# Kernel tuning notes

Measured on AMD Instinct MI355X. Metric: run time of the kernel, lower is better.

Reference implementation:

```python
import jax, jax.numpy as jnp
import numpy as np

N, E = 25000, 400000
HID, EDGE_F, DIM, HEADS, ADY = 128, 16, 3, 8, 64
INNER = int(1.25 * HID)          # 160
MSG_F = 2 * HID + EDGE_F + 1     # 273 (e3, relaxed=False -> 1 distance feature)


def silu(x):
    return x * jax.nn.sigmoid(x)


def ada_ln(x, y, W, b):
    # LayerNorm (no affine) + FiLM conditioning from y
    mu = jnp.mean(x, axis=-1, keepdims=True)
    var = jnp.var(x, axis=-1, keepdims=True)
    xn = (x - mu) * jax.lax.rsqrt(var + 1e-5)
    scale, shift = jnp.split(y @ W + b, 2, axis=-1)
    return xn * (1.0 + scale) + shift


def setup_inputs() -> dict:
    key = jax.random.key(0)
    ks = jax.random.split(key, 32)
    rn = lambda k, shp, s=0.05: (jax.random.normal(k, shp, jnp.float32) * s)
    inp = {
        'h': jax.random.normal(ks[0], (N, HID), jnp.float32),
        'coords': jax.random.normal(ks[1], (N, DIM), jnp.float32),
        'a': jax.random.normal(ks[2], (E, EDGE_F), jnp.float32),
        'y': jax.random.normal(ks[3], (N, ADY), jnp.float32),
        'res': jnp.zeros((N, HID), jnp.float32),
        'src': jax.random.randint(ks[4], (E,), 0, N, jnp.int32),
        'dst': jax.random.randint(ks[5], (E,), 0, N, jnp.int32),
        # edge MLP
        'We1': rn(ks[6], (MSG_F, INNER)), 'be1': jnp.zeros((INNER,), jnp.float32),
        'We2': rn(ks[7], (INNER, INNER)), 'be2': jnp.zeros((INNER,), jnp.float32),
        # coord head (xavier gain 0.001 -> tiny init)
        'Wc': rn(ks[8], (INNER, 1), 0.001),
        # attention/value/output heads
        'Wv': rn(ks[9], (INNER, HID)),
        'Wa': rn(ks[10], (INNER, HEADS)),
        'Wo': rn(ks[11], (HID, HID)),
        # node MLP
        'Wn1': rn(ks[12], (HID, INNER)), 'bn1': jnp.zeros((INNER,), jnp.float32),
        'Wn2': rn(ks[13], (INNER, HID)), 'bn2': jnp.zeros((HID,), jnp.float32),
        # adaptive LayerNorms (FiLM from y)
        'Wf1': rn(ks[14], (ADY, 2 * HID)), 'bf1': jnp.zeros((2 * HID,), jnp.float32),
        'Wf2': rn(ks[15], (ADY, 2 * HID)), 'bf2': jnp.zeros((2 * HID,), jnp.float32),
    }
    return inp


def reference(h, coords, a, y, res, src, dst,
              We1, be1, We2, be2, Wc, Wv, Wa, Wo,
              Wn1, bn1, Wn2, bn2, Wf1, bf1, Wf2, bf2):
    n = h.shape[0]
    heads = Wa.shape[1]
    # --- distance features (e3, relaxed=False): radial only ---
    xs, xd = coords[src], coords[dst]          # [E, 3]
    diffs = xs - xd
    radials = jnp.sum(diffs * diffs, axis=-1, keepdims=True)  # [E, 1]
    # --- edge MLP on gathered features ---
    f = jnp.concatenate([h[src], h[dst], radials, a], axis=-1)  # [E, 273]
    m = silu(f @ We1 + be1)
    m = silu(m @ We2 + be2)                    # [E, inner]
    # --- coordinate messages + scatter-sum to dst ---
    msg_x = (m @ Wc) * diffs / (jnp.sqrt(radials + 1e-5) + 1.0)  # [E, 3]
    coords_out = coords + jax.ops.segment_sum(msg_x, dst, num_segments=n)
    # --- edge softmax over incoming edges per dst node ---
    logits = m @ Wa                             # [E, heads]
    mx = jax.ops.segment_max(logits, dst, num_segments=n)
    ex = jnp.exp(logits - mx[dst])
    den = jax.ops.segment_sum(ex, dst, num_segments=n)
    w = ex / den[dst]                           # [E, heads]
    # --- weighted value aggregation ---
    vals = (m @ Wv).reshape(-1, heads, HID // heads) * w[:, :, None]
    h_agg = jax.ops.segment_sum(vals, dst, num_segments=n).reshape(n, HID)
    f2 = h_agg @ Wo
    res1 = res + f2
    h1 = ada_ln(h + f2, y, Wf1, bf1)
    f3 = silu(h1 @ Wn1 + bn1) @ Wn2 + bn2
    res2 = res1 + f3
    h2 = ada_ln(h1 + f3, y, Wf2, bf2)
    return (h2, coords_out, res2)
```

## Files before the change

kernel.cpp:

```cpp
#include <hip/hip_runtime.h>
#include <math.h>

#define N_NODES 25000
#define N_EDGES 400000
#define HID 128
#define EDGE_F 16
#define ADY 64
#define INNER 160
#define MSG_F 273
#define HEADS 8

#define OUT_CRD (N_NODES * HID)
#define OUT_RES (N_NODES * (HID + 3))

#define FLAG_OFF 0
#define DEN_OFF  256
#define CACC_OFF 800256
#define HAGG_OFF 1100288
#define HBF_OFF  13900288
#define YBF_OFF  20300288
#define BIAS_OFF 23500288
#define BW_OFF   23502592
#define MEMSET_BYTES 13900288

typedef unsigned short u16;
typedef unsigned int u32;
typedef unsigned long long u64;
typedef __attribute__((ext_vector_type(8))) short short8;
typedef __attribute__((ext_vector_type(4))) float f32x4;

__device__ __forceinline__ float bf2f(u16 v) {
    union { u32 u; float f; } x; x.u = ((u32)v) << 16; return x.f;
}
__device__ __forceinline__ u16 f2bf(float f) {
    union { float ff; u32 u; } x; x.ff = f;
    u32 u = x.u;
    u32 rounding = 0x7FFFu + ((u >> 16) & 1u);
    u += rounding;
    return (u16)(u >> 16);
}
__device__ __forceinline__ float silu(float z) {
    z = fminf(fmaxf(z, -30000.f), 30000.f);
    return z / (1.0f + __expf(-z));
}

template<bool F32> __device__ __forceinline__ float ldg1(const void* p, size_t i) {
    if (F32) return ((const float*)p)[i];
    return bf2f(((const u16*)p)[i]);
}
template<bool F32> __device__ __forceinline__ void stg1(void* p, size_t i, float v) {
    if (F32) ((float*)p)[i] = v;
    else     ((u16*)p)[i] = f2bf(v);
}
__device__ __forceinline__ float ldany(const void* p, size_t i, bool f32) {
    return f32 ? ((const float*)p)[i] : bf2f(((const u16*)p)[i]);
}
__device__ __forceinline__ void wave_lds_fence() {
    __builtin_amdgcn_wave_barrier();
    __builtin_amdgcn_s_waitcnt(0xc07f);
    __builtin_amdgcn_wave_barrier();
}

struct CvtArgs {
    const void* src[8];
    u64 dstoff[8];
    int n[8];
};
struct BwArgs {
    const void* We1; const void* We2; const void* Wv; const void* Wa;
    const void* Wc;  const void* Wo;  const void* Wn1; const void* Wn2;
    const void* Wf1; const void* Wf2;
    u64 b1, b2, b3, b4, b5, b6, b7, b8;
};

__global__ __launch_bounds__(256)
void preproc_kernel(const void* hsrc, int* flag, char* ws, CvtArgs args, BwArgs bwa)
{
    __shared__ float red[256];
    __shared__ int sflag;
    const int t = threadIdx.x;
    {
        const u16* p = (const u16*)hsrc;
        float mx = 0.f;
        for (int i = 0; i < 8; i++) {
            int idx = (t * 8 + i) * 97;
            float v = fabsf(bf2f(p[idx * 2]));
            mx = fmaxf(mx, v);
        }
        red[t] = mx;
        __syncthreads();
        for (int s = 128; s > 0; s >>= 1) {
            if (t < s) red[t] = fmaxf(red[t], red[t + s]);
            __syncthreads();
        }
        if (t == 0) {
            sflag = (red[0] > 1e10f || red[0] == 0.f) ? 1 : 0;
            if (blockIdx.x == 0) flag[0] = sflag;
        }
        __syncthreads();
    }
    const bool f32 = (sflag != 0);
    const int g = blockIdx.x * 256 + t;
    const int stride = gridDim.x * 256;

    for (int ten = 0; ten < 8; ten++) {
        const void* s = args.src[ten];
        u16* d = (u16*)(ws + args.dstoff[ten]);
        const int n = args.n[ten];
        if (f32) {
            const float* sf = (const float*)s;
            for (int i = g; i < n; i += stride) d[i] = f2bf(sf[i]);
        } else {
            const u16* su = (const u16*)s;
            for (int i = g; i < n; i += stride) d[i] = su[i];
        }
    }

    u16* b1 = (u16*)(ws + bwa.b1);
    u16* b2 = (u16*)(ws + bwa.b2);
    u16* b3 = (u16*)(ws + bwa.b3);
    u16* b4 = (u16*)(ws + bwa.b4);
    u16* b5 = (u16*)(ws + bwa.b5);
    u16* b6 = (u16*)(ws + bwa.b6);
    u16* b7 = (u16*)(ws + bwa.b7);
    u16* b8 = (u16*)(ws + bwa.b8);
    for (int i = g; i < 5*2*10*512; i += stride) {
        int tt = i >> 9, r = i & 511, l = r >> 3, j = r & 7;
        int c = tt / 20, ks = (tt / 10) % 2, nt = tt % 10;
        int k = c*64 + ks*32 + (l >> 4)*8 + j;
        int n = nt*16 + (l & 15);
        float v = 0.f;
        if (k < MSG_F)      v = ldany(bwa.We1, (size_t)k*INNER + n, f32);
        else if (k == 273)  v = ldany(bwa.We1, (size_t)256*INNER + n, f32);
        b1[i] = f2bf(v);
    }
    for (int i = g; i < 5*10*512; i += stride) {
        int tt = i >> 9, r = i & 511, l = r >> 3, j = r & 7;
        int k5 = tt / 10, nt = tt % 10;
        int k = k5*32 + (l >> 4)*8 + j;
        int n = nt*16 + (l & 15);
        b2[i] = f2bf(ldany(bwa.We2, (size_t)k*INNER + n, f32));
    }
    for (int i = g; i < 5*9*512; i += stride) {
        int tt = i >> 9, r = i & 511, l = r >> 3, j = r & 7;
        int k5 = tt / 9, nt = tt % 9;
        int k = k5*32 + (l >> 4)*8 + j;
        int n = nt*16 + (l & 15);
        float v = 0.f;
        if (n < 128)       v = ldany(bwa.Wv, (size_t)k*HID + n, f32);
        else if (n < 136)  v = ldany(bwa.Wa, (size_t)k*HEADS + (n-128), f32);
        else if (n == 136) v = ldany(bwa.Wc, (size_t)k, f32);
        b3[i] = f2bf(v);
    }
    for (int i = g; i < 4*8*512; i += stride) {
        int tt = i >> 9, r = i & 511, l = r >> 3, j = r & 7;
        int cks = tt / 8, nt = tt % 8;
        int k = cks*32 + (l >> 4)*8 + j;
        int n = nt*16 + (l & 15);
        b4[i] = f2bf(ldany(bwa.Wo, (size_t)k*HID + n, f32));
    }
    for (int i = g; i < 4*10*512; i += stride) {
        int tt = i >> 9, r = i & 511, l = r >> 3, j = r & 7;
        int cks = tt / 10, nt = tt % 10;
        int k = cks*32 + (l >> 4)*8 + j;
        int n = nt*16 + (l & 15);
        b5[i] = f2bf(ldany(bwa.Wn1, (size_t)k*INNER + n, f32));
    }
    for (int i = g; i < 5*8*512; i += stride) {
        int tt = i >> 9, r = i & 511, l = r >> 3, j = r & 7;
        int k5 = tt / 8, nt = tt % 8;
        int k = k5*32 + (l >> 4)*8 + j;
        int n = nt*16 + (l & 15);
        b6[i] = f2bf(ldany(bwa.Wn2, (size_t)k*HID + n, f32));
    }
    for (int i = g; i < 2*16*512; i += stride) {
        int tt = i >> 9, r = i & 511, l = r >> 3, j = r & 7;
        int ks = tt / 16, nt = tt % 16;
        int k = ks*32 + (l >> 4)*8 + j;
        int n = nt*16 + (l & 15);
        b7[i] = f2bf(ldany(bwa.Wf1, (size_t)k*256 + n, f32));
        b8[i] = f2bf(ldany(bwa.Wf2, (size_t)k*256 + n, f32));
    }
}

template<bool F32>
__device__ __forceinline__ void edge_body(
    const u16* __restrict__ hbf, const void* coords, const void* a,
    const int* __restrict__ src, const int* __restrict__ dst,
    const u16* __restrict__ We1P, const u16* __restrict__ We2P,
    const u16* __restrict__ W3P,
    const u16* __restrict__ cbe1, const u16* __restrict__ cbe2,
    float* __restrict__ den, float* __restrict__ hagg, float* __restrict__ cacc,
    u16* sPool, float* sdiff, float* srad, int* ssrc, int* sdstl)
{
    const int t   = threadIdx.x;
    const int w   = t >> 6;
    const int l   = t & 63;
    const int col = l & 15;
    const int q   = l >> 4;
    const int e0  = blockIdx.x * 64;
    const int l8  = l << 3;

    u16* sF  = sPool;
    u16* sM1 = sPool;
    u16* sM2 = sPool + 64*168;

    if (t < 64) {
        int e = e0 + t;
        int s = src[e], d = dst[e];
        ssrc[t] = s; sdstl[t] = d;
        float dx = ldg1<F32>(coords, (size_t)s*3+0) - ldg1<F32>(coords, (size_t)d*3+0);
        float dy = ldg1<F32>(coords, (size_t)s*3+1) - ldg1<F32>(coords, (size_t)d*3+1);
        float dz = ldg1<F32>(coords, (size_t)s*3+2) - ldg1<F32>(coords, (size_t)d*3+2);
        sdiff[t*4+0] = dx; sdiff[t*4+1] = dy; sdiff[t*4+2] = dz;
        float r2 = dx*dx + dy*dy + dz*dz;
        srad[t] = r2;
        sdiff[t*4+3] = 1.0f / (sqrtf(r2 + 1e-5f) + 1.0f);
    }
    __syncthreads();

    {
        int e = t >> 2, part = t & 3;
        int node_s = ssrc[e], node_d = sdstl[e];
        #pragma unroll
        for (int c = 0; c < 4; c++) {
            int node = (c < 2) ? node_s : node_d;
            int c0 = (c & 1) * 64 + part * 16;
            const uint4* gp = (const uint4*)(hbf + (size_t)node*HID + c0);
            *(uint4*)(&sF[e*360 + c*72 + part*16])     = gp[0];
            *(uint4*)(&sF[e*360 + c*72 + part*16 + 8]) = gp[1];
        }
        if (part < 2) {
            __align__(16) u16 tmp[16];
            #pragma unroll
            for (int j = 0; j < 16; j++) tmp[j] = 0;
            if (part == 0) {
                float r2 = srad[e];
                tmp[0] = f2bf(r2);
                for (int j = 0; j < 15; j++)
                    tmp[1+j] = f2bf(ldg1<F32>(a, (size_t)(e0+e)*EDGE_F + j));
            } else {
                tmp[0] = f2bf(ldg1<F32>(a, (size_t)(e0+e)*EDGE_F + 15));
                float r2 = srad[e];
                tmp[1] = f2bf(r2 - bf2f(f2bf(r2)));
            }
            *(uint4*)(&sF[e*360 + 4*72 + part*16])     = ((uint4*)tmp)[0];
            *(uint4*)(&sF[e*360 + 4*72 + part*16 + 8]) = ((uint4*)tmp)[1];
        }
    }
    __syncthreads();

    f32x4 acc1[10];
    #pragma unroll
    for (int nt = 0; nt < 10; nt++) {
        float v = bf2f(cbe1[nt*16 + col]);
        acc1[nt] = (f32x4){v, v, v, v};
    }
    const u16* fbase = &sF[(w*16 + col)*360];
    #pragma unroll
    for (int c = 0; c < 4; c++) {
        #pragma unroll
        for (int ks = 0; ks < 2; ks++) {
            short8 af = *(const short8*)(fbase + c*72 + ks*32 + q*8);
            const u16* B1 = We1P + (((c*2 + ks)*10) << 9) + l8;
            #pragma unroll
            for (int nt = 0; nt < 10; nt++) {
                short8 b = *(const short8*)(B1 + (nt << 9));
                acc1[nt] = __builtin_amdgcn_mfma_f32_16x16x32_bf16(af, b, acc1[nt], 0, 0, 0);
            }
        }
    }
    {
        short8 af = *(const short8*)(fbase + 4*72 + q*8);
        const u16* B1 = We1P + ((8*10) << 9) + l8;
        #pragma unroll
        for (int nt = 0; nt < 10; nt++) {
            short8 b = *(const short8*)(B1 + (nt << 9));
            acc1[nt] = __builtin_amdgcn_mfma_f32_16x16x32_bf16(af, b, acc1[nt], 0, 0, 0);
        }
    }
    __syncthreads();
    #pragma unroll
    for (int nt = 0; nt < 10; nt++)
        #pragma unroll
        for (int r = 0; r < 4; r++)
            sM1[(w*16 + q*4 + r)*168 + nt*16 + col] = f2bf(silu(acc1[nt][r]));
    __syncthreads();

    f32x4 acc2[10];
    #pragma unroll
    for (int nt = 0; nt < 10; nt++) {
        float v = bf2f(cbe2[nt*16 + col]);
        acc2[nt] = (f32x4){v, v, v, v};
    }
    const u16* m1base = &sM1[(w*16 + col)*168];
    #pragma unroll
    for (int k5 = 0; k5 < 5; k5++) {
        short8 af = *(const short8*)(m1base + k5*32 + q*8);
        const u16* B2 = We2P + ((k5*10) << 9) + l8;
        #pragma unroll
        for (int nt = 0; nt < 10; nt++) {
            short8 b = *(const short8*)(B2 + (nt << 9));
            acc2[nt] = __builtin_amdgcn_mfma_f32_16x16x32_bf16(af, b, acc2[nt], 0, 0, 0);
        }
    }
    #pragma unroll
    for (int nt = 0; nt < 10; nt++)
        #pragma unroll
        for (int r = 0; r < 4; r++)
            sM2[(w*16 + q*4 + r)*168 + nt*16 + col] = f2bf(silu(acc2[nt][r]));
    __syncthreads();

    f32x4 acc3[9];
    #pragma unroll
    for (int nt = 0; nt < 9; nt++) acc3[nt] = (f32x4){0.f, 0.f, 0.f, 0.f};
    const u16* m2base = &sM2[(w*16 + col)*168];
    #pragma unroll
    for (int k5 = 0; k5 < 5; k5++) {
        short8 af = *(const short8*)(m2base + k5*32 + q*8);
        const u16* B3 = W3P + ((k5*9) << 9) + l8;
        #pragma unroll
        for (int nt = 0; nt < 9; nt++) {
            short8 b = *(const short8*)(B3 + (nt << 9));
            acc3[nt] = __builtin_amdgcn_mfma_f32_16x16x32_bf16(af, b, acc3[nt], 0, 0, 0);
        }
    }

    int dstep[4];
    #pragma unroll
    for (int r = 0; r < 4; r++) dstep[r] = sdstl[w*16 + q*4 + r];

    float exv[4] = {0.f, 0.f, 0.f, 0.f};
    if (col < 8) {
        #pragma unroll
        for (int r = 0; r < 4; r++) {
            float ex = __expf(fminf(fmaxf(acc3[8][r], -30.f), 30.f));
            exv[r] = ex;
            atomicAdd(&den[(size_t)dstep[r]*8 + col], ex);
        }
    } else if (col == 8) {
        #pragma unroll
        for (int r = 0; r < 4; r++) {
            int idx = w*16 + q*4 + r;
            int dd = dstep[r];
            float invf = sdiff[idx*4 + 3];
            float lc = fminf(fmaxf(acc3[8][r], -1e6f), 1e6f) * invf;
            #pragma unroll
            for (int j = 0; j < 3; j++)
                atomicAdd(&cacc[(size_t)dd*3 + j], lc * sdiff[idx*4 + j]);
        }
    }
    #pragma unroll
    for (int nt = 0; nt < 8; nt++) {
        float ex0 = __shfl(exv[0], q*16 + nt);
        float ex1 = __shfl(exv[1], q*16 + nt);
        float ex2 = __shfl(exv[2], q*16 + nt);
        float ex3 = __shfl(exv[3], q*16 + nt);
        atomicAdd(&hagg[(size_t)dstep[0]*HID + nt*16 + col], acc3[nt][0] * ex0);
        atomicAdd(&hagg[(size_t)dstep[1]*HID + nt*16 + col], acc3[nt][1] * ex1);
        atomicAdd(&hagg[(size_t)dstep[2]*HID + nt*16 + col], acc3[nt][2] * ex2);
        atomicAdd(&hagg[(size_t)dstep[3]*HID + nt*16 + col], acc3[nt][3] * ex3);
    }
}

__global__ __launch_bounds__(256, 3)
void edge_kernel(const int* __restrict__ flag,
                 const u16* __restrict__ hbf, const void* coords, const void* a,
                 const int* __restrict__ src, const int* __restrict__ dst,
                 const u16* __restrict__ We1P, const u16* __restrict__ We2P,
                 const u16* __restrict__ W3P,
                 const u16* __restrict__ cbe1, const u16* __restrict__ cbe2,
                 float* __restrict__ den, float* __restrict__ hagg,
                 float* __restrict__ cacc)
{
    __shared__ __align__(16) u16 sPool[64*360];
    __shared__ float sdiff[64*4];
    __shared__ float srad[64];
    __shared__ int   ssrc[64];
    __shared__ int   sdstl[64];
    if (*flag)
        edge_body<true>(hbf, coords, a, src, dst, We1P, We2P, W3P, cbe1, cbe2,
                        den, hagg, cacc, sPool, sdiff, srad, ssrc, sdstl);
    else
        edge_body<false>(hbf, coords, a, src, dst, We1P, We2P, W3P, cbe1, cbe2,
                         den, hagg, cacc, sPool, sdiff, srad, ssrc, sdstl);
}

template<bool F32>
__device__ __forceinline__ void node_body(
    const u16* __restrict__ hbf, const void* res, const void* coords,
    const u16* __restrict__ ybf,
    const float* __restrict__ den, const float* __restrict__ hagg,
    const float* __restrict__ cacc,
    const u16* __restrict__ WoP, const u16* __restrict__ Wn1P,
    const u16* __restrict__ Wn2P, const u16* __restrict__ Wf1P,
    const u16* __restrict__ Wf2P,
    const u16* __restrict__ cbn1, const u16* __restrict__ cbn2,
    const u16* __restrict__ cbf1, const u16* __restrict__ cbf2,
    void* out, u16* sScr)
{
    const int t = threadIdx.x;
    const int w = t >> 6, l = t & 63, col = l & 15, q = l >> 4;
    const int nodew = blockIdx.x * 64 + w * 16;
    const int mynode = nodew + col;
    const bool okA = mynode < N_NODES;
    const int l8 = l << 3;
    u16* sc = sScr + w * 16 * 168;

    int gm[4]; bool okC[4];
    #pragma unroll
    for (int r = 0; r < 4; r++) { gm[r] = nodew + q*4 + r; okC[r] = gm[r] < N_NODES; }

    f32x4 aF2[8];
    #pragma unroll
    for (int nt = 0; nt < 8; nt++) aF2[nt] = (f32x4){0.f,0.f,0.f,0.f};
    #pragma unroll
    for (int c = 0; c < 2; c++) {
        #pragma unroll
        for (int ks = 0; ks < 2; ks++) {
            const int kbase = c*64 + ks*32 + q*8;
            union { u16 s[8]; short8 v; } u;
            if (okA) {
                float dd = den[(size_t)mynode*8 + (kbase >> 4)];
                float inv = dd > 0.f ? 1.f/dd : 0.f;
                const float4* gp = (const float4*)(hagg + (size_t)mynode*HID + kbase);
                float4 v0 = gp[0], v1 = gp[1];
                u.s[0]=f2bf(v0.x*inv); u.s[1]=f2bf(v0.y*inv); u.s[2]=f2bf(v0.z*inv); u.s[3]=f2bf(v0.w*inv);
                u.s[4]=f2bf(v1.x*inv); u.s[5]=f2bf(v1.y*inv); u.s[6]=f2bf(v1.z*inv); u.s[7]=f2bf(v1.w*inv);
            } else {
                #pragma unroll
                for (int j = 0; j < 8; j++) u.s[j] = 0;
            }
            const u16* B = WoP + (((c*2 + ks)*8) << 9) + l8;
            #pragma unroll
            for (int nt = 0; nt < 8; nt++) {
                short8 b = *(const short8*)(B + (nt << 9));
                aF2[nt] = __builtin_amdgcn_mfma_f32_16x16x32_bf16(u.v, b, aF2[nt], 0, 0, 0);
            }
        }
    }

    f32x4 aFl[16];
    #pragma unroll
    for (int nt = 0; nt < 16; nt++) {
        float v = bf2f(cbf1[nt*16 + col]);
        aFl[nt] = (f32x4){v,v,v,v};
    }
    #pragma unroll
    for (int ks = 0; ks < 2; ks++) {
        short8 af;
        if (okA) af = *(const short8*)(ybf + (size_t)mynode*ADY + ks*32 + q*8);
        else { union { u16 s[8]; short8 v; } z; for (int j=0;j<8;j++) z.s[j]=0; af = z.v; }
        const u16* B = Wf1P + ((ks*16) << 9) + l8;
        #pragma unroll
        for (int nt = 0; nt < 16; nt++) {
            short8 b = *(const short8*)(B + (nt << 9));
            aFl[nt] = __builtin_amdgcn_mfma_f32_16x16x32_bf16(af, b, aFl[nt], 0, 0, 0);
        }
    }

    float h1c[8][4], r1c[8][4];
    {
        float xv[8][4], s[4], ss[4];
        #pragma unroll
        for (int r = 0; r < 4; r++) { s[r] = 0.f; ss[r] = 0.f; }
        #pragma unroll
        for (int nt = 0; nt < 8; nt++)
            #pragma unroll
            for (int r = 0; r < 4; r++) {
                float hv = okC[r] ? bf2f(hbf[(size_t)gm[r]*HID + nt*16 + col]) : 0.f;
                float x = hv + aF2[nt][r];
                xv[nt][r] = x; s[r] += x; ss[r] += x*x;
            }
        #pragma unroll
        for (int r = 0; r < 4; r++)
            for (int off = 1; off <= 8; off <<= 1) {
                s[r]  += __shfl_xor(s[r], off);
                ss[r] += __shfl_xor(ss[r], off);
            }
        #pragma unroll
        for (int r = 0; r < 4; r++) {
            float mu = s[r] * (1.f/128.f);
            float var = ss[r] * (1.f/128.f) - mu*mu;
            float rs = rsqrtf(fmaxf(var, 0.f) + 1e-5f);
            #pragma unroll
            for (int nt = 0; nt < 8; nt++) {
                float h1 = (xv[nt][r]-mu)*rs*(1.f+aFl[nt][r]) + aFl[nt+8][r];
                h1c[nt][r] = h1;
                float rv = okC[r] ? ldg1<F32>(res, (size_t)gm[r]*HID + nt*16 + col) : 0.f;
                r1c[nt][r] = rv + aF2[nt][r];
                sc[(q*4 + r)*168 + nt*16 + col] = f2bf(h1);
            }
        }
    }
    wave_lds_fence();

    f32x4 aT[10];
    #pragma unroll
    for (int nt = 0; nt < 10; nt++) {
        float v = bf2f(cbn1[nt*16 + col]);
        aT[nt] = (f32x4){v,v,v,v};
    }
    #pragma unroll
    for (int c = 0; c < 2; c++) {
        #pragma unroll
        for (int ks = 0; ks < 2; ks++) {
            short8 af = *(const short8*)(sc + col*168 + c*64 + ks*32 + q*8);
            const u16* B = Wn1P + (((c*2 + ks)*10) << 9) + l8;
            #pragma unroll
            for (int nt = 0; nt < 10; nt++) {
                short8 b = *(const short8*)(B + (nt << 9));
                aT[nt] = __builtin_amdgcn_mfma_f32_16x16x32_bf16(af, b, aT[nt], 0, 0, 0);
            }
        }
    }
    wave_lds_fence();
    #pragma unroll
    for (int nt = 0; nt < 10; nt++)
        #pragma unroll
        for (int r = 0; r < 4; r++)
            sc[(q*4 + r)*168 + nt*16 + col] = f2bf(silu(aT[nt][r]));
    wave_lds_fence();

    f32x4 aF3[8];
    #pragma unroll
    for (int nt = 0; nt < 8; nt++) {
        float v = bf2f(cbn2[nt*16 + col]);
        aF3[nt] = (f32x4){v,v,v,v};
    }
    #pragma unroll
    for (int k5 = 0; k5 < 5; k5++) {
        short8 af = *(const short8*)(sc + col*168 + k5*32 + q*8);
        const u16* B = Wn2P + ((k5*8) << 9) + l8;
        #pragma unroll
        for (int nt = 0; nt < 8; nt++) {
            short8 b = *(const short8*)(B + (nt << 9));
            aF3[nt] = __builtin_amdgcn_mfma_f32_16x16x32_bf16(af, b, aF3[nt], 0, 0, 0);
        }
    }

    #pragma unroll
    for (int nt = 0; nt < 16; nt++) {
        float v = bf2f(cbf2[nt*16 + col]);
        aFl[nt] = (f32x4){v,v,v,v};
    }
    #pragma unroll
    for (int ks = 0; ks < 2; ks++) {
        short8 af;
        if (okA) af = *(const short8*)(ybf + (size_t)mynode*ADY + ks*32 + q*8);
        else { union { u16 s[8]; short8 v; } z; for (int j=0;j<8;j++) z.s[j]=0; af = z.v; }
        const u16* B = Wf2P + ((ks*16) << 9) + l8;
        #pragma unroll
        for (int nt = 0; nt < 16; nt++) {
            short8 b = *(const short8*)(B + (nt << 9));
            aFl[nt] = __builtin_amdgcn_mfma_f32_16x16x32_bf16(af, b, aFl[nt], 0, 0, 0);
        }
    }

    {
        float xv[8][4], s[4], ss[4];
        #pragma unroll
        for (int r = 0; r < 4; r++) { s[r] = 0.f; ss[r] = 0.f; }
        #pragma unroll
        for (int nt = 0; nt < 8; nt++)
            #pragma unroll
            for (int r = 0; r < 4; r++) {
                float x = h1c[nt][r] + aF3[nt][r];
                xv[nt][r] = x; s[r] += x; ss[r] += x*x;
            }
        #pragma unroll
        for (int r = 0; r < 4; r++)
            for (int off = 1; off <= 8; off <<= 1) {
                s[r]  += __shfl_xor(s[r], off);
                ss[r] += __shfl_xor(ss[r], off);
            }
        #pragma unroll
        for (int r = 0; r < 4; r++) {
            float mu = s[r] * (1.f/128.f);
            float var = ss[r] * (1.f/128.f) - mu*mu;
            float rs = rsqrtf(fmaxf(var, 0.f) + 1e-5f);
            if (okC[r]) {
                #pragma unroll
                for (int nt = 0; nt < 8; nt++) {
                    int n = nt*16 + col;
                    float h2 = (xv[nt][r]-mu)*rs*(1.f+aFl[nt][r]) + aFl[nt+8][r];
                    stg1<F32>(out, (size_t)gm[r]*HID + n, h2);
                    stg1<F32>(out, (size_t)OUT_RES + (size_t)gm[r]*HID + n,
                              r1c[nt][r] + aF3[nt][r]);
                }
            }
        }
    }

    if (q == 0 && okA) {
        #pragma unroll
        for (int j = 0; j < 3; j++)
            stg1<F32>(out, (size_t)OUT_CRD + (size_t)mynode*3 + j,
                      ldg1<F32>(coords, (size_t)mynode*3 + j) + cacc[(size_t)mynode*3 + j]);
    }
}

__global__ __launch_bounds__(256, 2)
void node_kernel(const int* __restrict__ flag,
                 const u16* __restrict__ hbf, const void* res, const void* coords,
                 const u16* __restrict__ ybf,
                 const float* __restrict__ den, const float* __restrict__ hagg,
                 const float* __restrict__ cacc,
                 const u16* __restrict__ WoP, const u16* __restrict__ Wn1P,
                 const u16* __restrict__ Wn2P, const u16* __restrict__ Wf1P,
                 const u16* __restrict__ Wf2P,
                 const u16* __restrict__ cbn1, const u16* __restrict__ cbn2,
                 const u16* __restrict__ cbf1, const u16* __restrict__ cbf2,
                 void* out)
{
    __shared__ __align__(16) u16 sScr[4 * 16 * 168];
    if (*flag)
        node_body<true>(hbf, res, coords, ybf, den, hagg, cacc, WoP, Wn1P, Wn2P,
                        Wf1P, Wf2P, cbn1, cbn2, cbf1, cbf2, out, sScr);
    else
        node_body<false>(hbf, res, coords, ybf, den, hagg, cacc, WoP, Wn1P, Wn2P,
                         Wf1P, Wf2P, cbn1, cbn2, cbf1, cbf2, out, sScr);
}

extern "C" void kernel_launch(void* const* d_in, const int* in_sizes, int n_in,
                              void* d_out, int out_size, void* d_ws, size_t ws_size,
                              hipStream_t stream)
{
    const void* h      = d_in[0];
    const void* coords = d_in[1];
    const void* a      = d_in[2];
    const void* y      = d_in[3];
    const void* res    = d_in[4];
    const int* src     = (const int*)d_in[5];
    const int* dst     = (const int*)d_in[6];

    char* ws = (char*)d_ws;
    int*   flag = (int*)(ws + FLAG_OFF);
    float* den  = (float*)(ws + DEN_OFF);
    float* cacc = (float*)(ws + CACC_OFF);
    float* hagg = (float*)(ws + HAGG_OFF);
    u16*   hbf  = (u16*)(ws + HBF_OFF);
    u16*   ybf  = (u16*)(ws + YBF_OFF);

    CvtArgs args;
    const int cvtn[8]   = {160, 160, 160, 128, 256, 256, N_NODES*HID, N_NODES*ADY};
    const int cvtsrc[8] = {8, 10, 16, 18, 20, 22, 0, 3};
    u64 boff[8];
    u64 bo = BIAS_OFF;
    for (int i = 0; i < 6; i++) {
        boff[i] = bo;
        bo += ((u64)cvtn[i] * 2 + 15) & ~(u64)15;
    }
    boff[6] = HBF_OFF;
    boff[7] = YBF_OFF;
    for (int i = 0; i < 8; i++) {
        args.src[i] = d_in[cvtsrc[i]];
        args.dstoff[i] = boff[i];
        args.n[i] = cvtn[i];
    }
    const u16* cbe1 = (const u16*)(ws + boff[0]);
    const u16* cbe2 = (const u16*)(ws + boff[1]);
    const u16* cbn1 = (const u16*)(ws + boff[2]);
    const u16* cbn2 = (const u16*)(ws + boff[3]);
    const u16* cbf1 = (const u16*)(ws + boff[4]);
    const u16* cbf2 = (const u16*)(ws + boff[5]);

    BwArgs bwa;
    bwa.We1 = d_in[7];  bwa.We2 = d_in[9];  bwa.Wv = d_in[12]; bwa.Wa = d_in[13];
    bwa.Wc  = d_in[11]; bwa.Wo  = d_in[14]; bwa.Wn1 = d_in[15]; bwa.Wn2 = d_in[17];
    bwa.Wf1 = d_in[19]; bwa.Wf2 = d_in[21];
    bwa.b1 = BW_OFF;
    bwa.b2 = bwa.b1 + (u64)5*2*10*512*2;
    bwa.b3 = bwa.b2 + (u64)5*10*512*2;
    bwa.b4 = bwa.b3 + (u64)5*9*512*2;
    bwa.b5 = bwa.b4 + (u64)4*8*512*2;
    bwa.b6 = bwa.b5 + (u64)4*10*512*2;
    bwa.b7 = bwa.b6 + (u64)5*8*512*2;
    bwa.b8 = bwa.b7 + (u64)2*16*512*2;
    const u16* We1P = (const u16*)(ws + bwa.b1);
    const u16* We2P = (const u16*)(ws + bwa.b2);
    const u16* W3P  = (const u16*)(ws + bwa.b3);
    const u16* WoP  = (const u16*)(ws + bwa.b4);
    const u16* Wn1P = (const u16*)(ws + bwa.b5);
    const u16* Wn2P = (const u16*)(ws + bwa.b6);
    const u16* Wf1P = (const u16*)(ws + bwa.b7);
    const u16* Wf2P = (const u16*)(ws + bwa.b8);

    hipMemsetAsync(d_ws, 0, MEMSET_BYTES, stream);

    preproc_kernel<<<256, 256, 0, stream>>>(h, flag, ws, args, bwa);

    edge_kernel<<<N_EDGES/64, 256, 0, stream>>>(flag, hbf, coords, a, src, dst,
                                                We1P, We2P, W3P, cbe1, cbe2,
                                                den, hagg, cacc);

    node_kernel<<<(N_NODES + 63)/64, 256, 0, stream>>>(
        flag, hbf, res, coords, ybf, den, hagg, cacc,
        WoP, Wn1P, Wn2P, Wf1P, Wf2P, cbn1, cbn2, cbf1, cbf2, d_out);
}
```

Baseline: 529.0 us.

## Sort edges by destination and merge consecutive same-node atomics

Adds a counting sort of edges by destination (a histogram in preproc, a single-block scan, then an atomic scatter into a permutation). The edge kernel now processes edges in that permuted order. Atomic adds for den, cacc and hagg are combined across a lane's four consecutive rows when they share the same dst. This is meant to cut global atomic traffic and contention and to improve locality of the scattered writes. In exchange it adds two kernel launches, a serial single-block scan, and indirect gathers of src/dst/a through the permutation. The order of float accumulation also becomes nondeterministic in a different way.

```diff
diff --git a/kernel.cpp b/kernel.cpp
--- a/kernel.cpp
+++ b/kernel.cpp
@@ -17,11 +17,12 @@
 #define DEN_OFF  256
 #define CACC_OFF 800256
 #define HAGG_OFF 1100288
-#define HBF_OFF  13900288
-#define YBF_OFF  20300288
-#define BIAS_OFF 23500288
-#define BW_OFF   23502592
-#define MEMSET_BYTES 13900288
+#define HIST_OFF 13900288
+#define MEMSET_BYTES 14000288
+#define HBF_OFF  14000288
+#define YBF_OFF  20400288
+#define BIAS_OFF 23600288
+#define BW_OFF   23602592
 
 typedef unsigned short u16;
 typedef unsigned int u32;
@@ -74,7 +75,8 @@
 };
 
 __global__ __launch_bounds__(256)
-void preproc_kernel(const void* hsrc, int* flag, char* ws, CvtArgs args, BwArgs bwa)
+void preproc_kernel(const void* hsrc, int* flag, char* ws, CvtArgs args, BwArgs bwa,
+                    const int* __restrict__ dste, int* __restrict__ hist)
 {
     __shared__ float red[256];
     __shared__ int sflag;
@@ -102,6 +104,9 @@
     const bool f32 = (sflag != 0);
     const int g = blockIdx.x * 256 + t;
     const int stride = gridDim.x * 256;
+
+    for (int e = g; e < N_EDGES; e += stride)
+        atomicAdd(&hist[dste[e]], 1);
 
     for (int ten = 0; ten < 8; ten++) {
         const void* s = args.src[ten];
@@ -183,15 +188,57 @@
     }
 }
 
+#define SCAN_CHUNK ((N_NODES + 255) / 256)
+__global__ __launch_bounds__(256)
+void scan_kernel(int* __restrict__ hist)
+{
+    __shared__ int part[256];
+    const int t = threadIdx.x;
+    const int base = t * SCAN_CHUNK;
+    int sum = 0;
+    for (int i = 0; i < SCAN_CHUNK; i++) {
+        int idx = base + i;
+        if (idx < N_NODES) sum += hist[idx];
+    }
+    part[t] = sum;
+    __syncthreads();
+    for (int off = 1; off < 256; off <<= 1) {
+        int v = (t >= off) ? part[t - off] : 0;
+        __syncthreads();
+        part[t] += v;
+        __syncthreads();
+    }
+    int run = part[t] - sum;
+    for (int i = 0; i < SCAN_CHUNK; i++) {
+        int idx = base + i;
+        if (idx < N_NODES) {
+            int hv = hist[idx];
+            hist[idx] = run;
+            run += hv;
+        }
+    }
+}
+
+__global__ __launch_bounds__(256)
+void scatter_kernel(const int* __restrict__ dste, int* __restrict__ offs,
+                    int* __restrict__ perm)
+{
+    for (int e = blockIdx.x * 256 + threadIdx.x; e < N_EDGES; e += gridDim.x * 256) {
+        int p = atomicAdd(&offs[dste[e]], 1);
+        perm[p] = e;
+    }
+}
+
 template<bool F32>
 __device__ __forceinline__ void edge_body(
     const u16* __restrict__ hbf, const void* coords, const void* a,
     const int* __restrict__ src, const int* __restrict__ dst,
+    const int* __restrict__ perm,
     const u16* __restrict__ We1P, const u16* __restrict__ We2P,
     const u16* __restrict__ W3P,
     const u16* __restrict__ cbe1, const u16* __restrict__ cbe2,
     float* __restrict__ den, float* __restrict__ hagg, float* __restrict__ cacc,
-    u16* sPool, float* sdiff, float* srad, int* ssrc, int* sdstl)
+    u16* sPool, float* sdiff, float* srad, int* ssrc, int* sdstl, int* seo)
 {
     const int t   = threadIdx.x;
     const int w   = t >> 6;
@@ -206,9 +253,9 @@
     u16* sM2 = sPool + 64*168;
 
     if (t < 64) {
-        int e = e0 + t;
-        int s = src[e], d = dst[e];
-        ssrc[t] = s; sdstl[t] = d;
+        int eo = perm[e0 + t];
+        int s = src[eo], d = dst[eo];
+        ssrc[t] = s; sdstl[t] = d; seo[t] = eo;
         float dx = ldg1<F32>(coords, (size_t)s*3+0) - ldg1<F32>(coords, (size_t)d*3+0);
         float dy = ldg1<F32>(coords, (size_t)s*3+1) - ldg1<F32>(coords, (size_t)d*3+1);
         float dz = ldg1<F32>(coords, (size_t)s*3+2) - ldg1<F32>(coords, (size_t)d*3+2);
@@ -234,13 +281,14 @@
             __align__(16) u16 tmp[16];
             #pragma unroll
             for (int j = 0; j < 16; j++) tmp[j] = 0;
+            int eo = seo[e];
             if (part == 0) {
                 float r2 = srad[e];
                 tmp[0] = f2bf(r2);
                 for (int j = 0; j < 15; j++)
-                    tmp[1+j] = f2bf(ldg1<F32>(a, (size_t)(e0+e)*EDGE_F + j));
+                    tmp[1+j] = f2bf(ldg1<F32>(a, (size_t)eo*EDGE_F + j));
             } else {
-                tmp[0] = f2bf(ldg1<F32>(a, (size_t)(e0+e)*EDGE_F + 15));
+                tmp[0] = f2bf(ldg1<F32>(a, (size_t)eo*EDGE_F + 15));
                 float r2 = srad[e];
                 tmp[1] = f2bf(r2 - bf2f(f2bf(r2)));
             }
@@ -332,34 +380,59 @@
 
     float exv[4] = {0.f, 0.f, 0.f, 0.f};
     if (col < 8) {
+        float dv[4];
         #pragma unroll
         for (int r = 0; r < 4; r++) {
             float ex = __expf(fminf(fmaxf(acc3[8][r], -30.f), 30.f));
-            exv[r] = ex;
-            atomicAdd(&den[(size_t)dstep[r]*8 + col], ex);
-        }
+            exv[r] = ex; dv[r] = ex;
+        }
+        float accu = dv[0]; int d = dstep[0];
+        #pragma unroll
+        for (int r = 1; r < 4; r++) {
+            if (dstep[r] == d) accu += dv[r];
+            else { atomicAdd(&den[(size_t)d*8 + col], accu); d = dstep[r]; accu = dv[r]; }
+        }
+        atomicAdd(&den[(size_t)d*8 + col], accu);
     } else if (col == 8) {
+        float cx[4], cy[4], cz[4];
         #pragma unroll
         for (int r = 0; r < 4; r++) {
             int idx = w*16 + q*4 + r;
-            int dd = dstep[r];
             float invf = sdiff[idx*4 + 3];
             float lc = fminf(fmaxf(acc3[8][r], -1e6f), 1e6f) * invf;
-            #pragma unroll
-            for (int j = 0; j < 3; j++)
-                atomicAdd(&cacc[(size_t)dd*3 + j], lc * sdiff[idx*4 + j]);
-        }
+            cx[r] = lc * sdiff[idx*4 + 0];
+            cy[r] = lc * sdiff[idx*4 + 1];
+            cz[r] = lc * sdiff[idx*4 + 2];
+        }
+        float ax = cx[0], ay = cy[0], az = cz[0]; int d = dstep[0];
+        #pragma unroll
+        for (int r = 1; r < 4; r++) {
+            if (dstep[r] == d) { ax += cx[r]; ay += cy[r]; az += cz[r]; }
+            else {
+                atomicAdd(&cacc[(size_t)d*3 + 0], ax);
+                atomicAdd(&cacc[(size_t)d*3 + 1], ay);
+                atomicAdd(&cacc[(size_t)d*3 + 2], az);
+                d = dstep[r]; ax = cx[r]; ay = cy[r]; az = cz[r];
+            }
+        }
+        atomicAdd(&cacc[(size_t)d*3 + 0], ax);
+        atomicAdd(&cacc[(size_t)d*3 + 1], ay);
+        atomicAdd(&cacc[(size_t)d*3 + 2], az);
     }
     #pragma unroll
     for (int nt = 0; nt < 8; nt++) {
-        float ex0 = __shfl(exv[0], q*16 + nt);
-        float ex1 = __shfl(exv[1], q*16 + nt);
-        float ex2 = __shfl(exv[2], q*16 + nt);
-        float ex3 = __shfl(exv[3], q*16 + nt);
-        atomicAdd(&hagg[(size_t)dstep[0]*HID + nt*16 + col], acc3[nt][0] * ex0);
-        atomicAdd(&hagg[(size_t)dstep[1]*HID + nt*16 + col], acc3[nt][1] * ex1);
-        atomicAdd(&hagg[(size_t)dstep[2]*HID + nt*16 + col], acc3[nt][2] * ex2);
-        atomicAdd(&hagg[(size_t)dstep[3]*HID + nt*16 + col], acc3[nt][3] * ex3);
+        float vv[4];
+        vv[0] = acc3[nt][0] * __shfl(exv[0], q*16 + nt);
+        vv[1] = acc3[nt][1] * __shfl(exv[1], q*16 + nt);
+        vv[2] = acc3[nt][2] * __shfl(exv[2], q*16 + nt);
+        vv[3] = acc3[nt][3] * __shfl(exv[3], q*16 + nt);
+        float accu = vv[0]; int d = dstep[0];
+        #pragma unroll
+        for (int r = 1; r < 4; r++) {
+            if (dstep[r] == d) accu += vv[r];
+            else { atomicAdd(&hagg[(size_t)d*HID + nt*16 + col], accu); d = dstep[r]; accu = vv[r]; }
+        }
+        atomicAdd(&hagg[(size_t)d*HID + nt*16 + col], accu);
     }
 }
 
@@ -367,6 +440,7 @@
 void edge_kernel(const int* __restrict__ flag,
                  const u16* __restrict__ hbf, const void* coords, const void* a,
                  const int* __restrict__ src, const int* __restrict__ dst,
+                 const int* __restrict__ perm,
                  const u16* __restrict__ We1P, const u16* __restrict__ We2P,
                  const u16* __restrict__ W3P,
                  const u16* __restrict__ cbe1, const u16* __restrict__ cbe2,
@@ -378,12 +452,13 @@
     __shared__ float srad[64];
     __shared__ int   ssrc[64];
     __shared__ int   sdstl[64];
+    __shared__ int   seo[64];
     if (*flag)
-        edge_body<true>(hbf, coords, a, src, dst, We1P, We2P, W3P, cbe1, cbe2,
-                        den, hagg, cacc, sPool, sdiff, srad, ssrc, sdstl);
+        edge_body<true>(hbf, coords, a, src, dst, perm, We1P, We2P, W3P, cbe1, cbe2,
+                        den, hagg, cacc, sPool, sdiff, srad, ssrc, sdstl, seo);
     else
-        edge_body<false>(hbf, coords, a, src, dst, We1P, We2P, W3P, cbe1, cbe2,
-                         den, hagg, cacc, sPool, sdiff, srad, ssrc, sdstl);
+        edge_body<false>(hbf, coords, a, src, dst, perm, We1P, We2P, W3P, cbe1, cbe2,
+                         den, hagg, cacc, sPool, sdiff, srad, ssrc, sdstl, seo);
 }
 
 template<bool F32>
@@ -639,6 +714,7 @@
     float* den  = (float*)(ws + DEN_OFF);
     float* cacc = (float*)(ws + CACC_OFF);
     float* hagg = (float*)(ws + HAGG_OFF);
+    int*   hist = (int*)(ws + HIST_OFF);
     u16*   hbf  = (u16*)(ws + HBF_OFF);
     u16*   ybf  = (u16*)(ws + YBF_OFF);
 
@@ -677,6 +753,7 @@
     bwa.b6 = bwa.b5 + (u64)4*10*512*2;
     bwa.b7 = bwa.b6 + (u64)5*8*512*2;
     bwa.b8 = bwa.b7 + (u64)2*16*512*2;
+    u64 perm_off = bwa.b8 + (u64)2*16*512*2;
     const u16* We1P = (const u16*)(ws + bwa.b1);
     const u16* We2P = (const u16*)(ws + bwa.b2);
     const u16* W3P  = (const u16*)(ws + bwa.b3);
@@ -685,12 +762,15 @@
     const u16* Wn2P = (const u16*)(ws + bwa.b6);
     const u16* Wf1P = (const u16*)(ws + bwa.b7);
     const u16* Wf2P = (const u16*)(ws + bwa.b8);
+    int* perm = (int*)(ws + perm_off);
 
     hipMemsetAsync(d_ws, 0, MEMSET_BYTES, stream);
 
-    preproc_kernel<<<256, 256, 0, stream>>>(h, flag, ws, args, bwa);
-
-    edge_kernel<<<N_EDGES/64, 256, 0, stream>>>(flag, hbf, coords, a, src, dst,
+    preproc_kernel<<<256, 256, 0, stream>>>(h, flag, ws, args, bwa, dst, hist);
+    scan_kernel<<<1, 256, 0, stream>>>(hist);
+    scatter_kernel<<<256, 256, 0, stream>>>(dst, hist, perm);
+
+    edge_kernel<<<N_EDGES/64, 256, 0, stream>>>(flag, hbf, coords, a, src, dst, perm,
                                                 We1P, We2P, W3P, cbe1, cbe2,
                                                 den, hagg, cacc);
 
```

After: 619.3 us. +17.1%, slower.
